# Performance work log

Measured on AMD Instinct MI355X. Metric: run time of the kernel, lower is better.

## Reference

```python
import jax, jax.numpy as jnp
import numpy as np

FEAT_DIM = 2048
HID = 256
N = 1024
NUM_CLASSES = 16
BN_EPS = 1e-5


def _batchnorm(x, gamma, beta):
    # training-mode BatchNorm1d: per-batch mean, biased variance
    m = x.mean(axis=0)
    v = x.var(axis=0)
    return gamma * (x - m) / jnp.sqrt(v + BN_EPS) + beta


def setup_inputs() -> dict:
    key = jax.random.key(0)
    ks = jax.random.split(key, 12)
    s1 = 1.0 / np.sqrt(FEAT_DIM)
    s2 = 1.0 / np.sqrt(HID)
    s3 = 1.0 / np.sqrt(2 * HID)
    return {
        "features": jax.random.normal(ks[0], (N, FEAT_DIM), dtype=jnp.float32),
        "labels": jax.random.randint(ks[1], (N,), 0, NUM_CLASSES, dtype=jnp.int32),
        # semantic disentangler
        "W1": jax.random.normal(ks[2], (FEAT_DIM, HID), dtype=jnp.float32) * s1,
        "b1": jnp.zeros((HID,), jnp.float32),
        "g1": jnp.ones((HID,), jnp.float32),
        "bt1": jnp.zeros((HID,), jnp.float32),
        "W2": jax.random.normal(ks[3], (HID, HID), dtype=jnp.float32) * s2,
        "b2": jnp.zeros((HID,), jnp.float32),
        "g2": jnp.ones((HID,), jnp.float32),
        "bt2": jnp.zeros((HID,), jnp.float32),
        # edge network: Linear(2H -> H), Linear(H -> 1)
        "We1": jax.random.normal(ks[4], (2 * HID, HID), dtype=jnp.float32) * s3,
        "bwe1": jnp.zeros((HID,), jnp.float32),
        "We2": jax.random.normal(ks[5], (HID, 1), dtype=jnp.float32) * s2,
        "bwe2": jnp.zeros((1,), jnp.float32),
    }


def reference(features, labels, W1, b1, g1, bt1, W2, b2, g2, bt2,
              We1, bwe1, We2, bwe2):
    # semantic disentangler: (Linear -> BN -> ReLU) x2
    h = jax.nn.relu(_batchnorm(features @ W1 + b1, g1, bt1))
    di = jax.nn.relu(_batchnorm(h @ W2 + b2, g2, bt2))  # [N, H]

    # EdgeNetwork all-pairs: Linear on concat([f_i, f_j]) splits into two GEMMs
    hi = di @ We1[:HID]   # [N, H] contribution of node i (first half of concat)
    hj = di @ We1[HID:]   # [N, H] contribution of node j (second half)
    pair = jax.nn.relu(hi[:, None, :] + hj[None, :, :] + bwe1)  # [N, N, H]
    logits = pair @ We2[:, 0] + bwe2[0]                          # [N, N]
    same_label = labels[:, None] == labels[None, :]
    off_diag = ~jnp.eye(N, dtype=bool)
    edge_weights = jnp.where(same_label & off_diag,
                             jax.nn.sigmoid(logits), 0.0)        # [N, N]

    # update_node_features: f_i + sum_j w_ij f_j / sum_j w_ij (if wsum > 0)
    weighted_sum = edge_weights @ di                 # [N, H] (w_ii == 0)
    wsum = edge_weights.sum(axis=1, keepdims=True)   # [N, 1]
    denom = jnp.where(wsum > 0, wsum, 1.0)
    updated = di + jnp.where(wsum > 0, weighted_sum / denom, 0.0)
    return updated
```

## Files before the change

kernel.cpp:

```cpp
#include <hip/hip_runtime.h>
#include <math.h>

#define N_PTS 1024
#define HID   256
#define FEAT  2048

typedef short bf16x8 __attribute__((ext_vector_type(8)));
typedef float f32x4  __attribute__((ext_vector_type(4)));

__device__ inline ushort f2bf(float f) {
    union { float f; unsigned u; } v; v.f = f;
    unsigned r = v.u + 0x7fff + ((v.u >> 16) & 1);
    return (ushort)(r >> 16);
}

__global__ __launch_bounds__(256) void prep(
    const float* __restrict__ features, const float* __restrict__ W1,
    const float* __restrict__ W2, const float* __restrict__ We1,
    ushort* __restrict__ Af, ushort* __restrict__ W1T,
    ushort* __restrict__ W2T, ushort* __restrict__ WeT,
    float* __restrict__ stats)
{
    const int tid = threadIdx.x;
    int b = blockIdx.x;
    if (b < 512) {
        if (b == 300)
            ((float4*)stats)[tid] = make_float4(0.f, 0.f, 0.f, 0.f);
        #pragma unroll
        for (int q = 0; q < 2; q++) {
            const size_t g = (size_t)b * 256 + tid + (size_t)q * 131072;
            float4 v0 = ((const float4*)features)[g * 2];
            float4 v1 = ((const float4*)features)[g * 2 + 1];
            bf16x8 o;
            o[0] = (short)f2bf(v0.x); o[1] = (short)f2bf(v0.y);
            o[2] = (short)f2bf(v0.z); o[3] = (short)f2bf(v0.w);
            o[4] = (short)f2bf(v1.x); o[5] = (short)f2bf(v1.y);
            o[6] = (short)f2bf(v1.z); o[7] = (short)f2bf(v1.w);
            ((bf16x8*)Af)[g] = o;
        }
        return;
    }
    __shared__ ushort Ts[64 * 72];
    const float* src; ushort* dst; int K;
    b -= 512;
    if (b < 128)      { src = W1;  dst = W1T; K = 2048; }
    else if (b < 144) { b -= 128; src = W2;  dst = W2T; K = 256; }
    else              { b -= 144; src = We1; dst = WeT; K = 512; }
    const int k0 = (b >> 2) * 64;
    const int n0 = (b & 3) * 64;
    #pragma unroll
    for (int p = 0; p < 4; p++) {
        const int c  = p * 256 + tid;
        const int r  = c >> 4;
        const int cq = c & 15;
        float4 v = *(const float4*)&src[(size_t)(k0 + r) * 256 + n0 + cq * 4];
        Ts[(cq * 4 + 0) * 72 + r] = f2bf(v.x);
        Ts[(cq * 4 + 1) * 72 + r] = f2bf(v.y);
        Ts[(cq * 4 + 2) * 72 + r] = f2bf(v.z);
        Ts[(cq * 4 + 3) * 72 + r] = f2bf(v.w);
    }
    __syncthreads();
    #pragma unroll
    for (int p = 0; p < 2; p++) {
        const int c    = p * 256 + tid;
        const int row  = c >> 3;
        const int col8 = c & 7;
        *(bf16x8*)&dst[(size_t)(n0 + row) * K + k0 + col8 * 8] =
            *(bf16x8*)&Ts[row * 72 + col8 * 8];
    }
}

__global__ __launch_bounds__(256) void gemm1p(
    const ushort* __restrict__ A, const ushort* __restrict__ B,
    float* __restrict__ Cp)
{
    __shared__ ushort As[64 * 72];
    __shared__ ushort Bs[64 * 72];
    const int tid  = threadIdx.x;
    const int lane = tid & 63;
    const int wave = tid >> 6;
    const int wy = wave >> 1, wx = wave & 1;
    const int quad = lane >> 4, l16 = lane & 15;
    const int mBase = blockIdx.y * 64;
    const int nBase = blockIdx.x * 64;
    const int kBeg  = blockIdx.z * 256;
    float* C = Cp + (size_t)blockIdx.z * (N_PTS * HID);

    f32x4 acc[2][2] = {};
    for (int ks = kBeg; ks < kBeg + 256; ks += 64) {
        #pragma unroll
        for (int p = 0; p < 2; p++) {
            const int c    = p * 256 + tid;
            const int row  = c >> 3;
            const int col8 = c & 7;
            *(bf16x8*)&As[row * 72 + col8 * 8] =
                *(const bf16x8*)&A[(size_t)(mBase + row) * FEAT + ks + col8 * 8];
            *(bf16x8*)&Bs[row * 72 + col8 * 8] =
                *(const bf16x8*)&B[(size_t)(nBase + row) * FEAT + ks + col8 * 8];
        }
        __syncthreads();
        #pragma unroll
        for (int kt = 0; kt < 64; kt += 32) {
            bf16x8 af[2], bfr[2];
            #pragma unroll
            for (int mi = 0; mi < 2; mi++)
                af[mi] = *(bf16x8*)&As[(wy * 32 + mi * 16 + l16) * 72 + kt + quad * 8];
            #pragma unroll
            for (int ni = 0; ni < 2; ni++)
                bfr[ni] = *(bf16x8*)&Bs[(wx * 32 + ni * 16 + l16) * 72 + kt + quad * 8];
            #pragma unroll
            for (int mi = 0; mi < 2; mi++)
                #pragma unroll
                for (int ni = 0; ni < 2; ni++)
                    acc[mi][ni] = __builtin_amdgcn_mfma_f32_16x16x32_bf16(
                        af[mi], bfr[ni], acc[mi][ni], 0, 0, 0);
        }
        __syncthreads();
    }
    #pragma unroll
    for (int mi = 0; mi < 2; mi++)
        #pragma unroll
        for (int ni = 0; ni < 2; ni++)
            #pragma unroll
            for (int e = 0; e < 4; e++) {
                const int gm = mBase + wy * 32 + mi * 16 + quad * 4 + e;
                const int gn = nBase + wx * 32 + ni * 16 + l16;
                C[(size_t)gm * HID + gn] = acc[mi][ni][e];
            }
}

__global__ __launch_bounds__(256) void reduce_stats(
    const float* __restrict__ Xp, float* __restrict__ X,
    float* __restrict__ sum, float* __restrict__ sq)
{
    const int c = threadIdx.x;
    const int r0 = blockIdx.x * 4;
    float s = 0.f, q = 0.f;
    for (int r = r0; r < r0 + 4; ++r) {
        float v = 0.f;
        #pragma unroll
        for (int z = 0; z < 8; z++)
            v += Xp[(size_t)z * (N_PTS * HID) + r * HID + c];
        X[r * HID + c] = v;
        s += v;
        q = fmaf(v, v, q);
    }
    unsafeAtomicAdd(&sum[c], s);
    unsafeAtomicAdd(&sq[c], q);
}

__global__ __launch_bounds__(256) void gemm2_fused(
    const float* __restrict__ A , const ushort* __restrict__ B ,
    float* __restrict__ C ,
    const float* __restrict__ sum1, const float* __restrict__ sq1,
    const float* __restrict__ g1, const float* __restrict__ bt1,
    float* __restrict__ sum2, float* __restrict__ sq2)
{
    __shared__ ushort As[64 * 72];
    __shared__ ushort Bs[64 * 72];
    __shared__ float sscale[HID];
    __shared__ float sshift[HID];
    __shared__ float csum[64];
    __shared__ float csq[64];
    const int tid  = threadIdx.x;
    const int lane = tid & 63;
    const int wave = tid >> 6;
    const int wy = wave >> 1, wx = wave & 1;
    const int quad = lane >> 4, l16 = lane & 15;
    const int mBase = blockIdx.y * 64;
    const int nBase = blockIdx.x * 64;

    {
        float m   = sum1[tid] * (1.f / 1024.f);
        float var = fmaf(-m, m, sq1[tid] * (1.f / 1024.f));
        float rstd = rsqrtf(var + 1e-5f);
        float sc = g1[tid] * rstd;
        sscale[tid] = sc;
        sshift[tid] = fmaf(-m, sc, bt1[tid]);
    }
    if (tid < 64) { csum[tid] = 0.f; csq[tid] = 0.f; }
    __syncthreads();

    f32x4 acc[2][2] = {};
    for (int ks = 0; ks < HID; ks += 64) {
        #pragma unroll
        for (int p = 0; p < 4; p++) {
            const int c  = p * 256 + tid;
            const int r  = c >> 4;
            const int cq = c & 15;
            const int k0 = ks + cq * 4;
            float4 av = *(const float4*)&A[(size_t)(mBase + r) * HID + k0];
            float v0 = fmaxf(fmaf(sscale[k0 + 0], av.x, sshift[k0 + 0]), 0.f);
            float v1 = fmaxf(fmaf(sscale[k0 + 1], av.y, sshift[k0 + 1]), 0.f);
            float v2 = fmaxf(fmaf(sscale[k0 + 2], av.z, sshift[k0 + 2]), 0.f);
            float v3 = fmaxf(fmaf(sscale[k0 + 3], av.w, sshift[k0 + 3]), 0.f);
            ushort4 ao;
            ao.x = f2bf(v0); ao.y = f2bf(v1); ao.z = f2bf(v2); ao.w = f2bf(v3);
            *(ushort4*)&As[r * 72 + cq * 4] = ao;
        }
        #pragma unroll
        for (int p = 0; p < 2; p++) {
            const int c    = p * 256 + tid;
            const int row  = c >> 3;
            const int col8 = c & 7;
            *(bf16x8*)&Bs[row * 72 + col8 * 8] =
                *(const bf16x8*)&B[(size_t)(nBase + row) * HID + ks + col8 * 8];
        }
        __syncthreads();
        #pragma unroll
        for (int kt = 0; kt < 64; kt += 32) {
            bf16x8 af[2], bfr[2];
            #pragma unroll
            for (int mi = 0; mi < 2; mi++)
                af[mi] = *(bf16x8*)&As[(wy * 32 + mi * 16 + l16) * 72 + kt + quad * 8];
            #pragma unroll
            for (int ni = 0; ni < 2; ni++)
                bfr[ni] = *(bf16x8*)&Bs[(wx * 32 + ni * 16 + l16) * 72 + kt + quad * 8];
            #pragma unroll
            for (int mi = 0; mi < 2; mi++)
                #pragma unroll
                for (int ni = 0; ni < 2; ni++)
                    acc[mi][ni] = __builtin_amdgcn_mfma_f32_16x16x32_bf16(
                        af[mi], bfr[ni], acc[mi][ni], 0, 0, 0);
        }
        __syncthreads();
    }

    float s[2] = {0.f, 0.f}, q[2] = {0.f, 0.f};
    #pragma unroll
    for (int mi = 0; mi < 2; mi++)
        #pragma unroll
        for (int ni = 0; ni < 2; ni++)
            #pragma unroll
            for (int e = 0; e < 4; e++) {
                const int gm = mBase + wy * 32 + mi * 16 + quad * 4 + e;
                const int gn = nBase + wx * 32 + ni * 16 + l16;
                float v = acc[mi][ni][e];
                C[(size_t)gm * HID + gn] = v;
                s[ni] += v;
                q[ni] = fmaf(v, v, q[ni]);
            }
    #pragma unroll
    for (int ni = 0; ni < 2; ni++) {
        float sv = s[ni], qv = q[ni];
        sv += __shfl_xor(sv, 16, 64); sv += __shfl_xor(sv, 32, 64);
        qv += __shfl_xor(qv, 16, 64); qv += __shfl_xor(qv, 32, 64);
        if (quad == 0) {
            atomicAdd(&csum[wx * 32 + ni * 16 + l16], sv);
            atomicAdd(&csq [wx * 32 + ni * 16 + l16], qv);
        }
    }
    __syncthreads();
    if (tid < 64) {
        unsafeAtomicAdd(&sum2[nBase + tid], csum[tid]);
        unsafeAtomicAdd(&sq2 [nBase + tid], csq[tid]);
    }
}

__global__ __launch_bounds__(256) void gemm_dual_bn(
    const float* __restrict__ A , const ushort* __restrict__ WeT,
    float* __restrict__ C1 , float* __restrict__ C2 ,
    const float* __restrict__ sum2, const float* __restrict__ sq2,
    const float* __restrict__ g2, const float* __restrict__ bt2,
    float* __restrict__ di)
{
    __shared__ ushort As[64 * 72];
    __shared__ ushort Bs[64 * 72];
    __shared__ float sscale[HID];
    __shared__ float sshift[HID];
    const int tid  = threadIdx.x;
    const int lane = tid & 63;
    const int wave = tid >> 6;
    const int wy = wave >> 1, wx = wave & 1;
    const int quad = lane >> 4, l16 = lane & 15;
    const int mBase = blockIdx.y * 64;
    const int nBase = blockIdx.x * 64;
    const int half  = blockIdx.z;
    float* C = half ? C2 : C1;
    const bool writeDi = (blockIdx.x == 0) && (half == 0);

    {
        float m   = sum2[tid] * (1.f / 1024.f);
        float var = fmaf(-m, m, sq2[tid] * (1.f / 1024.f));
        float rstd = rsqrtf(var + 1e-5f);
        float sc = g2[tid] * rstd;
        sscale[tid] = sc;
        sshift[tid] = fmaf(-m, sc, bt2[tid]);
    }
    __syncthreads();

    f32x4 acc[2][2] = {};
    for (int ks = 0; ks < HID; ks += 64) {
        #pragma unroll
        for (int p = 0; p < 4; p++) {
            const int c  = p * 256 + tid;
            const int r  = c >> 4;
            const int cq = c & 15;
            const int k0 = ks + cq * 4;
            float4 av = *(const float4*)&A[(size_t)(mBase + r) * HID + k0];
            float v0 = fmaxf(fmaf(sscale[k0 + 0], av.x, sshift[k0 + 0]), 0.f);
            float v1 = fmaxf(fmaf(sscale[k0 + 1], av.y, sshift[k0 + 1]), 0.f);
            float v2 = fmaxf(fmaf(sscale[k0 + 2], av.z, sshift[k0 + 2]), 0.f);
            float v3 = fmaxf(fmaf(sscale[k0 + 3], av.w, sshift[k0 + 3]), 0.f);
            if (writeDi)
                *(float4*)&di[(size_t)(mBase + r) * HID + k0] =
                    make_float4(v0, v1, v2, v3);
            ushort4 ao;
            ao.x = f2bf(v0); ao.y = f2bf(v1); ao.z = f2bf(v2); ao.w = f2bf(v3);
            *(ushort4*)&As[r * 72 + cq * 4] = ao;
        }
        #pragma unroll
        for (int p = 0; p < 2; p++) {
            const int c    = p * 256 + tid;
            const int row  = c >> 3;
            const int col8 = c & 7;
            *(bf16x8*)&Bs[row * 72 + col8 * 8] =
                *(const bf16x8*)&WeT[(size_t)(nBase + row) * 512 + half * 256 + ks + col8 * 8];
        }
        __syncthreads();
        #pragma unroll
        for (int kt = 0; kt < 64; kt += 32) {
            bf16x8 af[2], bfr[2];
            #pragma unroll
            for (int mi = 0; mi < 2; mi++)
                af[mi] = *(bf16x8*)&As[(wy * 32 + mi * 16 + l16) * 72 + kt + quad * 8];
            #pragma unroll
            for (int ni = 0; ni < 2; ni++)
                bfr[ni] = *(bf16x8*)&Bs[(wx * 32 + ni * 16 + l16) * 72 + kt + quad * 8];
            #pragma unroll
            for (int mi = 0; mi < 2; mi++)
                #pragma unroll
                for (int ni = 0; ni < 2; ni++)
                    acc[mi][ni] = __builtin_amdgcn_mfma_f32_16x16x32_bf16(
                        af[mi], bfr[ni], acc[mi][ni], 0, 0, 0);
        }
        __syncthreads();
    }
    #pragma unroll
    for (int mi = 0; mi < 2; mi++)
        #pragma unroll
        for (int ni = 0; ni < 2; ni++)
            #pragma unroll
            for (int e = 0; e < 4; e++) {
                const int gm = mBase + wy * 32 + mi * 16 + quad * 4 + e;
                const int gn = nBase + wx * 32 + ni * 16 + l16;
                C[(size_t)gm * HID + gn] = acc[mi][ni][e];
            }
}

__global__ __launch_bounds__(256) void pair_update2(
    const float* __restrict__ di, const float* __restrict__ hi,
    const float* __restrict__ hj, const float* __restrict__ bwe1,
    const float* __restrict__ We2, const float* __restrict__ bwe2,
    const int* __restrict__ labels, float* __restrict__ out)
{
    __shared__ int   slab[N_PTS];
    __shared__ int   list[N_PTS];
    __shared__ int   cnt;
    __shared__ float sacc[16][HID];
    __shared__ float swsum[16];
    const int i   = blockIdx.x;
    const int tid = threadIdx.x;
    const int pid = tid >> 4;
    const int l16 = tid & 15;

    if (tid == 0) cnt = 0;
    for (int t = tid; t < N_PTS; t += 256) slab[t] = labels[t];
    __syncthreads();
    const int myLab = slab[i];
    for (int t = tid; t < N_PTS; t += 256)
        if (slab[t] == myLab && t != i) list[atomicAdd(&cnt, 1)] = t;
    __syncthreads();
    const int n = cnt;

    const float4* hip4 = (const float4*)(hi + (size_t)i * HID) + l16 * 4;
    const float4* bw4  = (const float4*)bwe1 + l16 * 4;
    const float4* w24  = (const float4*)We2  + l16 * 4;
    float4 hb[4], w2[4];
    #pragma unroll
    for (int s = 0; s < 4; s++) {
        float4 a = hip4[s], b = bw4[s];
        hb[s] = make_float4(a.x + b.x, a.y + b.y, a.z + b.z, a.w + b.w);
        w2[s] = w24[s];
    }
    const float b2 = bwe2[0];

    float4 acc[4] = {};
    float wloc = 0.f;
    const int rounds = (n + 15) >> 4;
    for (int r = 0; r < rounds; ++r) {
        const int idx = r * 16 + pid;
        const bool valid = idx < n;
        const int jj = valid ? list[idx] : i;
        const float4* hv4 = (const float4*)(hj + (size_t)jj * HID) + l16 * 4;
        float4 hv[4];
        #pragma unroll
        for (int s = 0; s < 4; s++) hv[s] = hv4[s];
        float p = 0.f;
        #pragma unroll
        for (int s = 0; s < 4; s++) {
            p = fmaf(fmaxf(hb[s].x + hv[s].x, 0.f), w2[s].x, p);
            p = fmaf(fmaxf(hb[s].y + hv[s].y, 0.f), w2[s].y, p);
            p = fmaf(fmaxf(hb[s].z + hv[s].z, 0.f), w2[s].z, p);
            p = fmaf(fmaxf(hb[s].w + hv[s].w, 0.f), w2[s].w, p);
        }
        p += __shfl_xor(p, 1, 64);
        p += __shfl_xor(p, 2, 64);
        p += __shfl_xor(p, 4, 64);
        p += __shfl_xor(p, 8, 64);
        const float w = valid ? 1.f / (1.f + expf(-(p + b2))) : 0.f;
        const float4* dv4 = (const float4*)(di + (size_t)jj * HID) + l16 * 4;
        #pragma unroll
        for (int s = 0; s < 4; s++) {
            float4 d = dv4[s];
            acc[s].x = fmaf(w, d.x, acc[s].x);
            acc[s].y = fmaf(w, d.y, acc[s].y);
            acc[s].z = fmaf(w, d.z, acc[s].z);
            acc[s].w = fmaf(w, d.w, acc[s].w);
        }
        if (l16 == 0) wloc += w;
    }
    #pragma unroll
    for (int s = 0; s < 4; s++)
        ((float4*)&sacc[pid][l16 * 16])[s] = acc[s];
    if (l16 == 0) swsum[pid] = wloc;
    __syncthreads();

    float at = 0.f;
    #pragma unroll
    for (int g = 0; g < 16; g++) at += sacc[g][tid];
    float wt = 0.f;
    #pragma unroll
    for (int g = 0; g < 16; g++) wt += swsum[g];
    const float dval = di[(size_t)i * HID + tid];
    out[(size_t)i * HID + tid] = dval + (wt > 0.f ? at / wt : 0.f);
}

extern "C" void kernel_launch(void* const* d_in, const int* in_sizes, int n_in,
                              void* d_out, int out_size, void* d_ws, size_t ws_size,
                              hipStream_t stream)
{
    const float* features = (const float*)d_in[0];
    const int*   labels   = (const int*)d_in[1];
    const float* W1   = (const float*)d_in[2];
    const float* g1   = (const float*)d_in[4];
    const float* bt1  = (const float*)d_in[5];
    const float* W2   = (const float*)d_in[6];
    const float* g2   = (const float*)d_in[8];
    const float* bt2  = (const float*)d_in[9];
    const float* We1  = (const float*)d_in[10];
    const float* bwe1 = (const float*)d_in[11];
    const float* We2  = (const float*)d_in[12];
    const float* bwe2 = (const float*)d_in[13];
    float* out = (float*)d_out;

    float* ws    = (float*)d_ws;
    float* x1    = ws;
    float* hi    = ws + 262144;
    float* hj    = ws + 524288;
    float* stats = ws + 786432;
    float* x2    = ws + 787456;
    float* di    = ws + 1049600;
    float* x1p   = ws + 1311744;
    ushort* Af   = (ushort*)(ws + 3408896);
    ushort* W1T  = Af + 2097152;
    ushort* W2T  = W1T + 524288;
    ushort* WeT  = W2T + 65536;

    dim3 blk(256);
    prep<<<688, blk, 0, stream>>>(features, W1, W2, We1, Af, W1T, W2T, WeT,
                                  stats);
    gemm1p<<<dim3(4, 16, 8), blk, 0, stream>>>(Af, W1T, x1p);
    reduce_stats<<<256, blk, 0, stream>>>(x1p, x1, stats, stats + 256);
    gemm2_fused<<<dim3(4, 16, 1), blk, 0, stream>>>(x1, W2T, x2,
                                                    stats, stats + 256, g1, bt1,
                                                    stats + 512, stats + 768);
    gemm_dual_bn<<<dim3(4, 16, 2), blk, 0, stream>>>(x2, WeT, hi, hj,
                                                     stats + 512, stats + 768,
                                                     g2, bt2, di);
    pair_update2<<<N_PTS, blk, 0, stream>>>(di, hi, hj, bwe1, We2, bwe2,
                                            labels, out);
}
```

Before: 138.4 us.

## Replace split-K GEMM1 and reduce kernel with full-K GEMM emitting partial BN stats

Result: faster. 132.4 us, median of 2 (-4.3%).

```diff
diff --git a/kernel.cpp b/kernel.cpp
--- a/kernel.cpp
+++ b/kernel.cpp
@@ -18,14 +18,11 @@
     const float* __restrict__ features, const float* __restrict__ W1,
     const float* __restrict__ W2, const float* __restrict__ We1,
     ushort* __restrict__ Af, ushort* __restrict__ W1T,
-    ushort* __restrict__ W2T, ushort* __restrict__ WeT,
-    float* __restrict__ stats)
+    ushort* __restrict__ W2T, ushort* __restrict__ WeT)
 {
     const int tid = threadIdx.x;
     int b = blockIdx.x;
     if (b < 512) {
-        if (b == 300)
-            ((float4*)stats)[tid] = make_float4(0.f, 0.f, 0.f, 0.f);
         #pragma unroll
         for (int q = 0; q < 2; q++) {
             const size_t g = (size_t)b * 256 + tid + (size_t)q * 131072;
@@ -70,91 +67,67 @@
     }
 }
 
-__global__ __launch_bounds__(256) void gemm1p(
-    const ushort* __restrict__ A, const ushort* __restrict__ B,
-    float* __restrict__ Cp)
-{
-    __shared__ ushort As[64 * 72];
-    __shared__ ushort Bs[64 * 72];
+__global__ __launch_bounds__(256) void gemm1s(
+    const ushort* __restrict__ A , const ushort* __restrict__ B ,
+    float* __restrict__ X , float* __restrict__ statsP)
+{
+    __shared__ ushort As[16 * 136];
+    __shared__ ushort Bs[64 * 136];
     const int tid  = threadIdx.x;
     const int lane = tid & 63;
-    const int wave = tid >> 6;
-    const int wy = wave >> 1, wx = wave & 1;
+    const int w    = tid >> 6;
     const int quad = lane >> 4, l16 = lane & 15;
-    const int mBase = blockIdx.y * 64;
+    const int mBase = blockIdx.y * 16;
     const int nBase = blockIdx.x * 64;
-    const int kBeg  = blockIdx.z * 256;
-    float* C = Cp + (size_t)blockIdx.z * (N_PTS * HID);
-
-    f32x4 acc[2][2] = {};
-    for (int ks = kBeg; ks < kBeg + 256; ks += 64) {
-        #pragma unroll
-        for (int p = 0; p < 2; p++) {
+
+    f32x4 acc = {};
+    for (int ks = 0; ks < FEAT; ks += 128) {
+        {
+            const int row  = tid >> 4;
+            const int col8 = tid & 15;
+            *(bf16x8*)&As[row * 136 + col8 * 8] =
+                *(const bf16x8*)&A[(size_t)(mBase + row) * FEAT + ks + col8 * 8];
+        }
+        #pragma unroll
+        for (int p = 0; p < 4; p++) {
             const int c    = p * 256 + tid;
-            const int row  = c >> 3;
-            const int col8 = c & 7;
-            *(bf16x8*)&As[row * 72 + col8 * 8] =
-                *(const bf16x8*)&A[(size_t)(mBase + row) * FEAT + ks + col8 * 8];
-            *(bf16x8*)&Bs[row * 72 + col8 * 8] =
+            const int row  = c >> 4;
+            const int col8 = c & 15;
+            *(bf16x8*)&Bs[row * 136 + col8 * 8] =
                 *(const bf16x8*)&B[(size_t)(nBase + row) * FEAT + ks + col8 * 8];
         }
         __syncthreads();
         #pragma unroll
-        for (int kt = 0; kt < 64; kt += 32) {
-            bf16x8 af[2], bfr[2];
-            #pragma unroll
-            for (int mi = 0; mi < 2; mi++)
-                af[mi] = *(bf16x8*)&As[(wy * 32 + mi * 16 + l16) * 72 + kt + quad * 8];
-            #pragma unroll
-            for (int ni = 0; ni < 2; ni++)
-                bfr[ni] = *(bf16x8*)&Bs[(wx * 32 + ni * 16 + l16) * 72 + kt + quad * 8];
-            #pragma unroll
-            for (int mi = 0; mi < 2; mi++)
-                #pragma unroll
-                for (int ni = 0; ni < 2; ni++)
-                    acc[mi][ni] = __builtin_amdgcn_mfma_f32_16x16x32_bf16(
-                        af[mi], bfr[ni], acc[mi][ni], 0, 0, 0);
-        }
-        __syncthreads();
-    }
-    #pragma unroll
-    for (int mi = 0; mi < 2; mi++)
-        #pragma unroll
-        for (int ni = 0; ni < 2; ni++)
-            #pragma unroll
-            for (int e = 0; e < 4; e++) {
-                const int gm = mBase + wy * 32 + mi * 16 + quad * 4 + e;
-                const int gn = nBase + wx * 32 + ni * 16 + l16;
-                C[(size_t)gm * HID + gn] = acc[mi][ni][e];
-            }
-}
-
-__global__ __launch_bounds__(256) void reduce_stats(
-    const float* __restrict__ Xp, float* __restrict__ X,
-    float* __restrict__ sum, float* __restrict__ sq)
-{
-    const int c = threadIdx.x;
-    const int r0 = blockIdx.x * 4;
-    float s = 0.f, q = 0.f;
-    for (int r = r0; r < r0 + 4; ++r) {
-        float v = 0.f;
-        #pragma unroll
-        for (int z = 0; z < 8; z++)
-            v += Xp[(size_t)z * (N_PTS * HID) + r * HID + c];
-        X[r * HID + c] = v;
-        s += v;
-        q = fmaf(v, v, q);
-    }
-    unsafeAtomicAdd(&sum[c], s);
-    unsafeAtomicAdd(&sq[c], q);
+        for (int kt = 0; kt < 128; kt += 32) {
+            bf16x8 af = *(bf16x8*)&As[l16 * 136 + kt + quad * 8];
+            bf16x8 bf = *(bf16x8*)&Bs[(w * 16 + l16) * 136 + kt + quad * 8];
+            acc = __builtin_amdgcn_mfma_f32_16x16x32_bf16(af, bf, acc, 0, 0, 0);
+        }
+        __syncthreads();
+    }
+    float sv = 0.f, qv = 0.f;
+    #pragma unroll
+    for (int e = 0; e < 4; e++) {
+        const int gm = mBase + quad * 4 + e;
+        const int gn = nBase + w * 16 + l16;
+        X[(size_t)gm * HID + gn] = acc[e];
+        sv += acc[e];
+        qv = fmaf(acc[e], acc[e], qv);
+    }
+    sv += __shfl_xor(sv, 16, 64); sv += __shfl_xor(sv, 32, 64);
+    qv += __shfl_xor(qv, 16, 64); qv += __shfl_xor(qv, 32, 64);
+    if (quad == 0) {
+        const int c = nBase + w * 16 + l16;
+        statsP[blockIdx.y * 512 + c]       = sv;
+        statsP[blockIdx.y * 512 + 256 + c] = qv;
+    }
 }
 
 __global__ __launch_bounds__(256) void gemm2_fused(
     const float* __restrict__ A , const ushort* __restrict__ B ,
-    float* __restrict__ C ,
-    const float* __restrict__ sum1, const float* __restrict__ sq1,
+    float* __restrict__ C , const float* __restrict__ statsP,
     const float* __restrict__ g1, const float* __restrict__ bt1,
-    float* __restrict__ sum2, float* __restrict__ sq2)
+    float* __restrict__ stats2P)
 {
     __shared__ ushort As[64 * 72];
     __shared__ ushort Bs[64 * 72];
@@ -171,8 +144,14 @@
     const int nBase = blockIdx.x * 64;
 
     {
-        float m   = sum1[tid] * (1.f / 1024.f);
-        float var = fmaf(-m, m, sq1[tid] * (1.f / 1024.f));
+        float s1 = 0.f, q1 = 0.f;
+        #pragma unroll 8
+        for (int y = 0; y < 64; y++) {
+            s1 += statsP[y * 512 + tid];
+            q1 += statsP[y * 512 + 256 + tid];
+        }
+        float m   = s1 * (1.f / 1024.f);
+        float var = fmaf(-m, m, q1 * (1.f / 1024.f));
         float rstd = rsqrtf(var + 1e-5f);
         float sc = g1[tid] * rstd;
         sscale[tid] = sc;
@@ -252,15 +231,15 @@
     }
     __syncthreads();
     if (tid < 64) {
-        unsafeAtomicAdd(&sum2[nBase + tid], csum[tid]);
-        unsafeAtomicAdd(&sq2 [nBase + tid], csq[tid]);
+        stats2P[blockIdx.y * 512 + nBase + tid]       = csum[tid];
+        stats2P[blockIdx.y * 512 + 256 + nBase + tid] = csq[tid];
     }
 }
 
 __global__ __launch_bounds__(256) void gemm_dual_bn(
     const float* __restrict__ A , const ushort* __restrict__ WeT,
     float* __restrict__ C1 , float* __restrict__ C2 ,
-    const float* __restrict__ sum2, const float* __restrict__ sq2,
+    const float* __restrict__ stats2P,
     const float* __restrict__ g2, const float* __restrict__ bt2,
     float* __restrict__ di)
 {
@@ -280,8 +259,14 @@
     const bool writeDi = (blockIdx.x == 0) && (half == 0);
 
     {
-        float m   = sum2[tid] * (1.f / 1024.f);
-        float var = fmaf(-m, m, sq2[tid] * (1.f / 1024.f));
+        float s2 = 0.f, q2 = 0.f;
+        #pragma unroll
+        for (int y = 0; y < 16; y++) {
+            s2 += stats2P[y * 512 + tid];
+            q2 += stats2P[y * 512 + 256 + tid];
+        }
+        float m   = s2 * (1.f / 1024.f);
+        float var = fmaf(-m, m, q2 * (1.f / 1024.f));
         float rstd = rsqrtf(var + 1e-5f);
         float sc = g2[tid] * rstd;
         sscale[tid] = sc;
@@ -454,30 +439,26 @@
     const float* bwe2 = (const float*)d_in[13];
     float* out = (float*)d_out;
 
-    float* ws    = (float*)d_ws;
-    float* x1    = ws;
-    float* hi    = ws + 262144;
-    float* hj    = ws + 524288;
-    float* stats = ws + 786432;
-    float* x2    = ws + 787456;
-    float* di    = ws + 1049600;
-    float* x1p   = ws + 1311744;
-    ushort* Af   = (ushort*)(ws + 3408896);
+    float* ws      = (float*)d_ws;
+    float* x1      = ws;
+    float* hi      = ws + 262144;
+    float* hj      = ws + 524288;
+    float* x2      = ws + 786432;
+    float* di      = ws + 1048576;
+    float* statsP  = ws + 1310720;
+    float* stats2P = ws + 1343488;
+    ushort* Af   = (ushort*)(ws + 1351680);
     ushort* W1T  = Af + 2097152;
     ushort* W2T  = W1T + 524288;
     ushort* WeT  = W2T + 65536;
 
     dim3 blk(256);
-    prep<<<688, blk, 0, stream>>>(features, W1, W2, We1, Af, W1T, W2T, WeT,
-                                  stats);
-    gemm1p<<<dim3(4, 16, 8), blk, 0, stream>>>(Af, W1T, x1p);
-    reduce_stats<<<256, blk, 0, stream>>>(x1p, x1, stats, stats + 256);
-    gemm2_fused<<<dim3(4, 16, 1), blk, 0, stream>>>(x1, W2T, x2,
-                                                    stats, stats + 256, g1, bt1,
-                                                    stats + 512, stats + 768);
+    prep<<<688, blk, 0, stream>>>(features, W1, W2, We1, Af, W1T, W2T, WeT);
+    gemm1s<<<dim3(4, 64), blk, 0, stream>>>(Af, W1T, x1, statsP);
+    gemm2_fused<<<dim3(4, 16), blk, 0, stream>>>(x1, W2T, x2, statsP,
+                                                 g1, bt1, stats2P);
     gemm_dual_bn<<<dim3(4, 16, 2), blk, 0, stream>>>(x2, WeT, hi, hj,
-                                                     stats + 512, stats + 768,
-                                                     g2, bt2, di);
+                                                     stats2P, g2, bt2, di);
     pair_update2<<<N_PTS, blk, 0, stream>>>(di, hi, hj, bwe1, We2, bwe2,
                                             labels, out);
 }
```
